# Performance work log

Measured on AMD Instinct MI355X. Metric: run time of the kernel, lower is better.

The kernel has to match this reference:

```python
import jax, jax.numpy as jnp
from jax import lax
import numpy as np

B, V, H, K, E = 256, 30000, 512, 200, 300
SH_ALPHA = 20.0
REC_W = 0.7
N_ITERS = 100       # fixed iteration budget (original caps at 5000; convergence check freezes updates)
STOP_THR = 0.005
BN_EPS = 1e-3


def setup_inputs() -> dict:
    key = jax.random.key(0)
    ks = jax.random.split(key, 8)
    n = lambda k, shape, scale: (jax.random.normal(k, shape, jnp.float32) * scale)
    return {
        "bows": jax.random.uniform(ks[0], (B, V), jnp.float32),
        "W1": n(ks[1], (H, V), 0.01),
        "b1": jnp.zeros((H,), jnp.float32),
        "W2": n(ks[2], (K, H), 0.05),
        "b2": jnp.zeros((K,), jnp.float32),
        "gamma": jnp.ones((K,), jnp.float32),
        "beta": jnp.zeros((K,), jnp.float32),
        "word_emb": n(ks[3], (V, E), 0.1),
        "topic_emb": n(ks[4], (K, E), 0.1),
    }


def _l2norm(x):
    return x / jnp.maximum(jnp.linalg.norm(x, axis=1, keepdims=True), 1e-12)


def _sinkhorn(cost, kernel, a, b):
    # a: [K,B], b: [V,B], kernel: [K,V]
    u0 = jnp.ones_like(a) / a.shape[0]
    v0 = jnp.ones_like(b)

    def body(carry, i):
        u, v, err = carry
        active = err > STOP_THR
        # u = a / (kernel @ (b / (u^T kernel)^T))
        u1 = a / (kernel @ (b / (u.T @ kernel).T))

        def check(_):
            v1 = b / (kernel.T @ u1)
            u2 = a / (kernel @ v1)
            bb = v1 * (kernel.T @ u2)
            e = jnp.max(jnp.sum(jnp.abs(bb - b), axis=0))
            return u2, v1, e

        # original does the v-refresh + err check when steps % 20 == 1 (steps = i+1)
        u1, v1, e1 = lax.cond(i % 20 == 0, check, lambda _: (u1, v, err), None)
        u = jnp.where(active, u1, u)
        v = jnp.where(active, v1, v)
        err = jnp.where(active, e1, err)
        return (u, v, err), None

    (u, v, _), _ = lax.scan(jax.checkpoint(body), (u0, v0, jnp.asarray(1.0, a.dtype)),
                            jnp.arange(N_ITERS))
    # per-document sinkhorn cost: sum_k u * ((kernel*cost) @ v)
    return jnp.sum(u * ((kernel * cost) @ v), axis=0)  # [B]


def reference(bows, W1, b1, W2, b2, gamma, beta, word_emb, topic_emb):
    # encoder (training-mode BN with batch stats; dropout disabled for determinism)
    h = jax.nn.relu(bows @ W1.T + b1)                      # [B,H]
    z = h @ W2.T + b2                                      # [B,K]
    mu = jnp.mean(z, axis=0)
    var = jnp.var(z, axis=0)                               # biased, as torch BN uses
    zn = gamma * (z - mu) / jnp.sqrt(var + BN_EPS) + beta
    doc_topic = jax.nn.softmax(zn, axis=1)                 # [B,K]

    topic_word = _l2norm(topic_emb) @ _l2norm(word_emb).T  # [K,V]
    cost = 1.0 - topic_word
    kernel = jnp.exp(-cost * SH_ALPHA)

    doc_word = jax.nn.softmax(bows, axis=1)                # [B,V]
    sinkhorn_loss = _sinkhorn(cost, kernel, doc_topic.T, doc_word.T).mean()

    rec_log_probs = jax.nn.log_softmax(doc_topic @ topic_word, axis=1)  # [B,V]
    reconstruction_loss = -(rec_log_probs * bows).sum(axis=1).mean()
    return REC_W * reconstruction_loss, sinkhorn_loss
```

## Files before the change

kernel.cpp:

```cpp
#include <hip/hip_runtime.h>
#include <math.h>

#define CDIV(a,b) (((a)+(b)-1)/(b))

typedef unsigned short u16;
typedef unsigned long long u64;
typedef __attribute__((ext_vector_type(8))) short bf16x8;
typedef __attribute__((ext_vector_type(4))) float f32x4;

constexpr int Bn = 256;
constexpr int Vn = 30000;
constexpr int Hn = 512;
constexpr int Kn = 200;
constexpr int En = 300;
constexpr int E3 = 320;
constexpr int Kp = 224;
constexpr int Vc = 224;
constexpr int NCH = 136;
constexpr int CPX = NCH / 8;
constexpr int Vpad = NCH * Vc;
constexpr int KQ = 50;
constexpr int SW1 = 120;
constexpr int KSL = 256;
constexpr float ALPHA  = 20.0f;
constexpr float RECW   = 0.7f;
constexpr float THRC   = 0.005f;
constexpr float EPS_BN = 1e-3f;
constexpr int   NIT    = 100;

__device__ __forceinline__ float bf2f(u16 h) {
  union { unsigned u; float f; } c; c.u = (unsigned)h << 16; return c.f;
}
__device__ __forceinline__ u16 f2bf(float f) {
  union { float f; unsigned u; } c; c.f = f;
  return (u16)((c.u + 0x7fffu + ((c.u >> 16) & 1u)) >> 16);
}
__device__ __forceinline__ bf16x8 load8bf(const float* p) {
  float4 a = *(const float4*)p, b = *(const float4*)(p + 4);
  bf16x8 r;
  r[0] = (short)f2bf(a.x); r[1] = (short)f2bf(a.y);
  r[2] = (short)f2bf(a.z); r[3] = (short)f2bf(a.w);
  r[4] = (short)f2bf(b.x); r[5] = (short)f2bf(b.y);
  r[6] = (short)f2bf(b.z); r[7] = (short)f2bf(b.w);
  return r;
}

template<int MODE>
__global__ __launch_bounds__(256, 2)
void fusedAB(const u16* __restrict__ kernT, const u16* __restrict__ kernA,
             const u16* __restrict__ ub, const u16* __restrict__ bmb,
             u16* __restrict__ wout, const u16* __restrict__ win,
             u16* __restrict__ tpart, float* __restrict__ errp,
             const int* __restrict__ frozen)
{
  if (MODE != 3 && frozen[0]) return;
  const int bid = blockIdx.x;
  const int xcd = bid & 7, wid = bid >> 3;
  const int c = xcd * CPX + (wid >> 2), g = wid & 3;
  const int v0 = c * Vc, b0 = g * 64;
  const int tid = threadIdx.x;
  const int wv = tid >> 6, l = tid & 63, l15 = l & 15, lg = l >> 4;
  const int rloc = wv * 16 + l15;
  const int bcol = b0 + rloc;
  __shared__ u16 wlds[64 * Vc];
  char* wbase = (char*)wlds;
  const int sw = (rloc & 3) << 4;

  if (MODE != 3) {
    bf16x8 uf[7];
    {
      const u16* up = ub + (size_t)bcol * Kp + lg * 8;
#pragma unroll
      for (int ks = 0; ks < 7; ++ks) uf[ks] = *(const bf16x8*)(up + ks * 32);
    }
    float e = 0.f;
    for (int vt = 0; vt < Vc / 16; ++vt) {
      const u16* ktp = kernT + (size_t)(v0 + vt * 16 + l15) * Kp + lg * 8;
      f32x4 acc = {0.f, 0.f, 0.f, 0.f};
#pragma unroll
      for (int ks = 0; ks < 7; ++ks) {
        bf16x8 kf = *(const bf16x8*)(ktp + ks * 32);
        acc = __builtin_amdgcn_mfma_f32_16x16x32_bf16(kf, uf[ks], acc, 0, 0, 0);
      }
      const int vbase = v0 + vt * 16 + lg * 4;
      const size_t po = (size_t)bcol * Vpad + vbase;
      u64 bq = __builtin_nontemporal_load((const u64*)(bmb + po));
      if (MODE == 2) {
        u64 wq = __builtin_nontemporal_load((const u64*)(win + po));
#pragma unroll
        for (int r = 0; r < 4; ++r) {
          float bm = bf2f((u16)(bq >> (16 * r)));
          float wv_ = bf2f((u16)(wq >> (16 * r)));
          e += fabsf(wv_ * acc[r] - bm);
        }
      } else {
        u64 wq = 0;
#pragma unroll
        for (int r = 0; r < 4; ++r) {
          float bm = bf2f((u16)(bq >> (16 * r)));
          float w = (vbase + r < Vn) ? bm / acc[r] : 0.f;
          wq |= (u64)f2bf(w) << (16 * r);
        }
        *(u64*)(wbase + rloc * (Vc * 2) + ((vt * 32 + lg * 8) ^ sw)) = wq;
        if (MODE == 1) __builtin_nontemporal_store(wq, (u64*)(wout + po));
      }
    }
    if (MODE == 2) {
      e += __shfl_xor(e, 16, 64);
      e += __shfl_xor(e, 32, 64);
      if (l < 16) errp[c * Bn + bcol] = e;
      return;
    }
    __syncthreads();
  }

  f32x4 accB[13];
#pragma unroll
  for (int mt = 0; mt < 13; ++mt) accB[mt] = (f32x4){0.f, 0.f, 0.f, 0.f};
  for (int vs = 0; vs < Vc / 32; ++vs) {
    bf16x8 wf;
    if (MODE == 3) {
      union { u64 q[2]; bf16x8 v; } wu;
      const u64* wp = (const u64*)(win + (size_t)bcol * Vpad + v0 + vs * 32 + lg * 8);
      wu.q[0] = __builtin_nontemporal_load(wp);
      wu.q[1] = __builtin_nontemporal_load(wp + 1);
      wf = wu.v;
    } else {
      wf = *(const bf16x8*)(wbase + rloc * (Vc * 2) + (((vs * 32 + lg * 8) * 2) ^ sw));
    }
    const u16* kap = kernA + (size_t)l15 * Vpad + v0 + vs * 32 + lg * 8;
#pragma unroll
    for (int mt = 0; mt < 13; ++mt) {
      bf16x8 af = *(const bf16x8*)(kap + (size_t)mt * 16 * Vpad);
      accB[mt] = __builtin_amdgcn_mfma_f32_16x16x32_bf16(af, wf, accB[mt], 0, 0, 0);
    }
  }
#pragma unroll
  for (int mt = 0; mt < 13; ++mt) {
    const int kq = mt * 4 + lg;
    if (kq < KQ) {
      u64 q = (u64)f2bf(accB[mt][0])
            | ((u64)f2bf(accB[mt][1]) << 16)
            | ((u64)f2bf(accB[mt][2]) << 32)
            | ((u64)f2bf(accB[mt][3]) << 48);
      __builtin_nontemporal_store(q, (u64*)(tpart + (((size_t)c * KQ + kq) * Bn + bcol) * 4));
    }
  }
}

__global__ __launch_bounds__(256, 2)
void reconMF(const u16* __restrict__ costT, const u16* __restrict__ dtb,
             u16* __restrict__ rbuf)
{
  const int c = blockIdx.x, g = blockIdx.y;
  const int v0 = c * Vc, b0 = g * 64;
  const int tid = threadIdx.x;
  const int wv = tid >> 6, l = tid & 63, l15 = l & 15, lg = l >> 4;
  const int bcol = b0 + wv * 16 + l15;
  bf16x8 uf[7];
  {
    const u16* up = dtb + (size_t)bcol * Kp + lg * 8;
#pragma unroll
    for (int ks = 0; ks < 7; ++ks) uf[ks] = *(const bf16x8*)(up + ks * 32);
  }
  for (int vt = 0; vt < Vc / 16; ++vt) {
    const u16* ktp = costT + (size_t)(v0 + vt * 16 + l15) * Kp + lg * 8;
    f32x4 acc = {0.f, 0.f, 0.f, 0.f};
#pragma unroll
    for (int ks = 0; ks < 7; ++ks) {
      bf16x8 kf = *(const bf16x8*)(ktp + ks * 32);
      acc = __builtin_amdgcn_mfma_f32_16x16x32_bf16(kf, uf[ks], acc, 0, 0, 0);
    }
    const int vbase = v0 + vt * 16 + lg * 4;
    u64 q = 0;
#pragma unroll
    for (int r = 0; r < 4; ++r) q |= (u64)f2bf(1.f - acc[r]) << (16 * r);
    *(u64*)(rbuf + (size_t)bcol * Vpad + vbase) = q;
  }
}

__global__ __launch_bounds__(256)
void gemmTW(const u16* __restrict__ nth, const u16* __restrict__ ntl,
            const u16* __restrict__ nwh, const u16* __restrict__ nwl,
            u16* __restrict__ kern_bf, u16* __restrict__ kc_bf,
            u16* __restrict__ cost_bf)
{
  const int n0 = blockIdx.x * 64;
  const int tid = threadIdx.x;
  const int wv = tid >> 6, l = tid & 63, l15 = l & 15, lg = l >> 4;
  const int n = n0 + wv * 16 + l15;
  const bool nok = n < Vn;
  f32x4 acc[14];
#pragma unroll
  for (int mt = 0; mt < 14; ++mt) acc[mt] = (f32x4){0.f, 0.f, 0.f, 0.f};
  for (int kc = 0; kc < E3; kc += 32) {
    bf16x8 bh = {0,0,0,0,0,0,0,0}, bl = {0,0,0,0,0,0,0,0};
    if (nok) {
      const size_t o = (size_t)n * E3 + kc + lg * 8;
      bh = *(const bf16x8*)(nwh + o);
      bl = *(const bf16x8*)(nwl + o);
    }
#pragma unroll
    for (int mt = 0; mt < 14; ++mt) {
      const size_t ao = (size_t)(mt * 16 + l15) * E3 + kc + lg * 8;
      bf16x8 ah = *(const bf16x8*)(nth + ao);
      bf16x8 al = *(const bf16x8*)(ntl + ao);
      acc[mt] = __builtin_amdgcn_mfma_f32_16x16x32_bf16(ah, bh, acc[mt], 0, 0, 0);
      acc[mt] = __builtin_amdgcn_mfma_f32_16x16x32_bf16(ah, bl, acc[mt], 0, 0, 0);
      acc[mt] = __builtin_amdgcn_mfma_f32_16x16x32_bf16(al, bh, acc[mt], 0, 0, 0);
    }
  }
#pragma unroll
  for (int mt = 0; mt < 14; ++mt) {
#pragma unroll
    for (int r = 0; r < 4; ++r) {
      int k = mt * 16 + lg * 4 + r;
      float cf = 1.f - acc[mt][r];
      float kf = expf(-ALPHA * cf);
      size_t o = (size_t)k * Vpad + n;
      kern_bf[o] = f2bf(kf);
      kc_bf[o]   = f2bf(kf * cf);
      cost_bf[o] = f2bf(cf);
    }
  }
}

__global__ __launch_bounds__(256)
void gemmW1(const float* __restrict__ A, const float* __restrict__ B,
            float* __restrict__ part)
{
  const int bid = blockIdx.x;
  const int xcd = bid & 7, t = bid >> 3;
  const int s = xcd * 15 + (t >> 3);
  const int nx = t & 7;
  const int n0 = nx * 64, k0 = s * KSL;
  const int tid = threadIdx.x;
  const int wv = tid >> 6, l = tid & 63, l15 = l & 15, lg = l >> 4;
  f32x4 acc[4][4];
#pragma unroll
  for (int i = 0; i < 4; ++i)
#pragma unroll
    for (int j = 0; j < 4; ++j) acc[i][j] = (f32x4){0.f, 0.f, 0.f, 0.f};

  bf16x8 aA[4], bA[4], aB[4], bB[4];

#define LDW1(KC, AF, BF)                                                        \
  { const int kk_ = (KC) + lg * 8;                                              \
    const bool ok_ = kk_ < Vn;                                                  \
    _Pragma("unroll")                                                           \
    for (int mt = 0; mt < 4; ++mt) {                                            \
      const int m_ = wv * 64 + mt * 16 + l15;                                   \
      AF[mt] = ok_ ? load8bf(A + (size_t)m_ * Vn + kk_) : (bf16x8){0,0,0,0,0,0,0,0}; \
    }                                                                           \
    _Pragma("unroll")                                                           \
    for (int nt = 0; nt < 4; ++nt) {                                            \
      const int n_ = n0 + nt * 16 + l15;                                        \
      BF[nt] = ok_ ? load8bf(B + (size_t)n_ * Vn + kk_) : (bf16x8){0,0,0,0,0,0,0,0}; \
    } }

#define FMAW1(AF, BF)                                                           \
  _Pragma("unroll")                                                             \
  for (int mt = 0; mt < 4; ++mt)                                                \
    _Pragma("unroll")                                                           \
    for (int nt = 0; nt < 4; ++nt)                                              \
      acc[mt][nt] = __builtin_amdgcn_mfma_f32_16x16x32_bf16(AF[mt], BF[nt], acc[mt][nt], 0, 0, 0);

  LDW1(k0, aA, bA);
#pragma unroll
  for (int step = 0; step < KSL / 32; ++step) {
    if ((step & 1) == 0) {
      if (step + 1 < KSL / 32) LDW1(k0 + (step + 1) * 32, aB, bB);
      FMAW1(aA, bA);
    } else {
      if (step + 1 < KSL / 32) LDW1(k0 + (step + 1) * 32, aA, bA);
      FMAW1(aB, bB);
    }
  }
#undef LDW1
#undef FMAW1

#pragma unroll
  for (int mt = 0; mt < 4; ++mt)
#pragma unroll
    for (int nt = 0; nt < 4; ++nt)
#pragma unroll
      for (int r = 0; r < 4; ++r) {
        const int m = wv * 64 + mt * 16 + lg * 4 + r;
        const int n = n0 + nt * 16 + l15;
        part[(size_t)s * (Bn * Hn) + (size_t)m * Hn + n] = acc[mt][nt][r];
      }
}

__global__ void transposeK(const u16* __restrict__ src, u16* __restrict__ dst)
{
  __shared__ u16 t[32][33];
  int tx = threadIdx.x & 31, ty = threadIdx.x >> 5;
  int v0 = blockIdx.x * 32, k0 = blockIdx.y * 32;
#pragma unroll
  for (int r = 0; r < 4; ++r) t[ty + 8 * r][tx] = src[(size_t)(k0 + ty + 8 * r) * Vpad + v0 + tx];
  __syncthreads();
#pragma unroll
  for (int r = 0; r < 4; ++r) dst[(size_t)(v0 + ty + 8 * r) * Kp + k0 + tx] = t[tx][ty + 8 * r];
}

__global__ void convTemb(const float* __restrict__ temb, const float* __restrict__ rnT,
                         u16* __restrict__ nth, u16* __restrict__ ntl)
{
  int k = blockIdx.x, e = threadIdx.x;
  float v = (k < Kn && e < En) ? temb[(size_t)k * En + e] * rnT[k] : 0.f;
  u16 hi = f2bf(v);
  nth[(size_t)k * E3 + e] = hi;
  ntl[(size_t)k * E3 + e] = f2bf(v - bf2f(hi));
}

__global__ void convWemb(const float* __restrict__ wemb, const float* __restrict__ rnW,
                         u16* __restrict__ nwh, u16* __restrict__ nwl)
{
  for (size_t idx = (size_t)blockIdx.x * 256 + threadIdx.x; idx < (size_t)Vn * E3;
       idx += (size_t)gridDim.x * 256) {
    int v = (int)(idx / E3), e = (int)(idx - (size_t)v * E3);
    float x = (e < En) ? wemb[(size_t)v * En + e] * rnW[v] : 0.f;
    u16 hi = f2bf(x);
    nwh[idx] = hi;
    nwl[idx] = f2bf(x - bf2f(hi));
  }
}

__global__ __launch_bounds__(256)
void gemm_nt(const float* __restrict__ A, const float* __restrict__ Bm,
             float* __restrict__ P, int M, int N, int Kd)
{
  const int S = gridDim.z, s = blockIdx.z;
  const int k0 = (int)((long long)Kd * s / S);
  const int k1 = (int)((long long)Kd * (s + 1) / S);
  const int m0 = blockIdx.y * 64, n0 = blockIdx.x * 64;
  __shared__ float As[16][68];
  __shared__ float Bs[16][68];
  const int tid = threadIdx.x;
  const int tx = tid & 15, ty = tid >> 4;
  const int lrow = tid >> 2, lkg = (tid & 3) * 4;
  const int mi = m0 + lrow, ni = n0 + lrow;
  float acc[4][4] = {};
  for (int kc = k0; kc < k1; kc += 16) {
    float4 a4 = {0.f, 0.f, 0.f, 0.f}, b4 = {0.f, 0.f, 0.f, 0.f};
    if (mi < M) a4 = *(const float4*)&A[(size_t)mi * Kd + kc + lkg];
    if (ni < N) b4 = *(const float4*)&Bm[(size_t)ni * Kd + kc + lkg];
    As[lkg + 0][lrow] = a4.x; As[lkg + 1][lrow] = a4.y;
    As[lkg + 2][lrow] = a4.z; As[lkg + 3][lrow] = a4.w;
    Bs[lkg + 0][lrow] = b4.x; Bs[lkg + 1][lrow] = b4.y;
    Bs[lkg + 2][lrow] = b4.z; Bs[lkg + 3][lrow] = b4.w;
    __syncthreads();
#pragma unroll
    for (int kk = 0; kk < 16; ++kk) {
      float4 av = *(const float4*)&As[kk][ty * 4];
      float4 bv = *(const float4*)&Bs[kk][tx * 4];
      float a_[4] = {av.x, av.y, av.z, av.w};
      float b_[4] = {bv.x, bv.y, bv.z, bv.w};
#pragma unroll
      for (int i = 0; i < 4; ++i)
#pragma unroll
        for (int j = 0; j < 4; ++j)
          acc[i][j] += a_[i] * b_[j];
    }
    __syncthreads();
  }
  const size_t base = (size_t)s * M * N;
#pragma unroll
  for (int i = 0; i < 4; ++i) {
    int m = m0 + ty * 4 + i;
    if (m >= M) continue;
#pragma unroll
    for (int j = 0; j < 4; ++j) {
      int n = n0 + tx * 4 + j;
      if (n < N) P[base + (size_t)m * N + n] = acc[i][j];
    }
  }
}

__global__ void rowNorms(const float* __restrict__ X, float* __restrict__ rn, int R, int C)
{
  int wv = threadIdx.x >> 6, lane = threadIdx.x & 63;
  int r = blockIdx.x * 4 + wv;
  if (r >= R) return;
  float s = 0.f;
  for (int c = lane; c < C; c += 64) { float x = X[(size_t)r * C + c]; s += x * x; }
#pragma unroll
  for (int m = 32; m; m >>= 1) s += __shfl_xor(s, m, 64);
  if (lane == 0) rn[r] = 1.f / fmaxf(sqrtf(s), 1e-12f);
}

__global__ void epiH(const float* __restrict__ P, const float* __restrict__ b1,
                     float* __restrict__ h, int S)
{
  int i = blockIdx.x * blockDim.x + threadIdx.x;
  if (i >= Bn * Hn) return;
  float v = b1[i & (Hn - 1)];
#pragma unroll 8
  for (int s = 0; s < S; ++s) v += P[(size_t)s * Bn * Hn + i];
  h[i] = fmaxf(v, 0.f);
}

__global__ void bnStats(const float* __restrict__ P, const float* __restrict__ b2,
                        float* __restrict__ mu, float* __restrict__ ivar, int S)
{
  int k = blockIdx.x, b = threadIdx.x;
  float z = b2[k];
  for (int s = 0; s < S; ++s) z += P[((size_t)s * Bn + b) * Kn + k];
  __shared__ float r1[256], r2[256];
  r1[b] = z; r2[b] = z * z; __syncthreads();
  for (int st = 128; st; st >>= 1) {
    if (b < st) { r1[b] += r1[b + st]; r2[b] += r2[b + st]; }
    __syncthreads();
  }
  if (b == 0) {
    float m = r1[0] / Bn, v = r2[0] / Bn - (r1[0] / Bn) * (r1[0] / Bn);
    mu[k] = m; ivar[k] = rsqrtf(v + EPS_BN);
  }
}

__global__ void bnSoftmax(const float* __restrict__ P, const float* __restrict__ b2,
                          const float* __restrict__ mu, const float* __restrict__ ivar,
                          const float* __restrict__ gamma, const float* __restrict__ beta,
                          float* __restrict__ a, u16* __restrict__ dtb, int S)
{
  int b = blockIdx.x, k = threadIdx.x;
  float zn = -1e30f;
  if (k < Kn) {
    float z = b2[k];
    for (int s = 0; s < S; ++s) z += P[((size_t)s * Bn + b) * Kn + k];
    zn = gamma[k] * (z - mu[k]) * ivar[k] + beta[k];
  }
  __shared__ float red[256];
  red[k] = zn; __syncthreads();
  for (int st = 128; st; st >>= 1) { if (k < st) red[k] = fmaxf(red[k], red[k + st]); __syncthreads(); }
  float mx = red[0]; __syncthreads();
  float e = (k < Kn) ? expf(zn - mx) : 0.f;
  red[k] = e; __syncthreads();
  for (int st = 128; st; st >>= 1) { if (k < st) red[k] += red[k + st]; __syncthreads(); }
  float dt = e / red[0];
  if (k < Kn) a[(size_t)k * Bn + b] = dt;
  if (k < Kp) dtb[(size_t)b * Kp + k] = (k < Kn) ? f2bf(dt) : (u16)0;
}

__global__ __launch_bounds__(512)
void rowSoftmax2(const float* __restrict__ bows, u16* __restrict__ bmb)
{
  int b = blockIdx.x, t = threadIdx.x;
  const float4* row = (const float4*)(bows + (size_t)b * Vn);
  __shared__ float red[512];
  float mx = -1e30f;
  for (int v4 = t; v4 < Vn / 4; v4 += 512) {
    float4 x = row[v4];
    mx = fmaxf(mx, fmaxf(fmaxf(x.x, x.y), fmaxf(x.z, x.w)));
  }
  red[t] = mx; __syncthreads();
  for (int st = 256; st; st >>= 1) { if (t < st) red[t] = fmaxf(red[t], red[t + st]); __syncthreads(); }
  mx = red[0]; __syncthreads();
  float sum = 0.f;
  for (int v4 = t; v4 < Vn / 4; v4 += 512) {
    float4 x = row[v4];
    sum += expf(x.x - mx) + expf(x.y - mx) + expf(x.z - mx) + expf(x.w - mx);
  }
  red[t] = sum; __syncthreads();
  for (int st = 256; st; st >>= 1) { if (t < st) red[t] += red[t + st]; __syncthreads(); }
  float inv = 1.f / red[0];
  for (int v4 = t; v4 < Vn / 4; v4 += 512) {
    float4 x = row[v4];
    u64 q = (u64)f2bf(expf(x.x - mx) * inv)
          | ((u64)f2bf(expf(x.y - mx) * inv) << 16)
          | ((u64)f2bf(expf(x.z - mx) * inv) << 32)
          | ((u64)f2bf(expf(x.w - mx) * inv) << 48);
    *(u64*)(bmb + (size_t)b * Vpad + v4 * 4) = q;
  }
  for (int p = t; p < (Vpad - Vn) / 4; p += 512)
    *(u64*)(bmb + (size_t)b * Vpad + Vn + p * 4) = 0;
}

__global__ void initU2(u16* __restrict__ ub)
{
  int b = blockIdx.x, k = threadIdx.x;
  ub[(size_t)b * Kp + k] = (k < Kn) ? f2bf(1.f / Kn) : (u16)0;
}

__global__ __launch_bounds__(256)
void updateU2(const u16* __restrict__ tpart, const float* __restrict__ a,
              u16* __restrict__ ub, const int* __restrict__ frozen)
{
  if (frozen[0]) return;
  const int kq = blockIdx.x >> 2, bq = blockIdx.x & 3;
  const int cg = threadIdx.x >> 6, bloc = threadIdx.x & 63;
  const int b = bq * 64 + bloc;
  f32x4 t = {0.f, 0.f, 0.f, 0.f};
  for (int c = cg * (NCH / 4); c < (cg + 1) * (NCH / 4); ++c) {
    u64 qd = __builtin_nontemporal_load(
        (const u64*)(tpart + (((size_t)c * KQ + kq) * Bn + b) * 4));
    t[0] += bf2f((u16)qd);         t[1] += bf2f((u16)(qd >> 16));
    t[2] += bf2f((u16)(qd >> 32)); t[3] += bf2f((u16)(qd >> 48));
  }
  __shared__ f32x4 red[4][64];
  red[cg][bloc] = t;
  __syncthreads();
  if (cg == 0) {
    f32x4 s = red[0][bloc];
#pragma unroll
    for (int gg = 1; gg < 4; ++gg) {
      f32x4 o = red[gg][bloc];
      s[0] += o[0]; s[1] += o[1]; s[2] += o[2]; s[3] += o[3];
    }
    const int k0 = kq * 4;
    u64 q = (u64)f2bf(a[(size_t)(k0 + 0) * Bn + b] / s[0])
          | ((u64)f2bf(a[(size_t)(k0 + 1) * Bn + b] / s[1]) << 16)
          | ((u64)f2bf(a[(size_t)(k0 + 2) * Bn + b] / s[2]) << 32)
          | ((u64)f2bf(a[(size_t)(k0 + 3) * Bn + b] / s[3]) << 48);
    *(u64*)(ub + (size_t)b * Kp + k0) = q;
  }
}

__global__ __launch_bounds__(256)
void sumT(const u16* __restrict__ tpart, float* __restrict__ t2)
{
  const int kq = blockIdx.x >> 2, bq = blockIdx.x & 3;
  const int cg = threadIdx.x >> 6, bloc = threadIdx.x & 63;
  const int b = bq * 64 + bloc;
  f32x4 t = {0.f, 0.f, 0.f, 0.f};
  for (int c = cg * (NCH / 4); c < (cg + 1) * (NCH / 4); ++c) {
    u64 qd = __builtin_nontemporal_load(
        (const u64*)(tpart + (((size_t)c * KQ + kq) * Bn + b) * 4));
    t[0] += bf2f((u16)qd);         t[1] += bf2f((u16)(qd >> 16));
    t[2] += bf2f((u16)(qd >> 32)); t[3] += bf2f((u16)(qd >> 48));
  }
  __shared__ f32x4 red[4][64];
  red[cg][bloc] = t;
  __syncthreads();
  if (cg == 0) {
    f32x4 s = red[0][bloc];
#pragma unroll
    for (int gg = 1; gg < 4; ++gg) {
      f32x4 o = red[gg][bloc];
      s[0] += o[0]; s[1] += o[1]; s[2] += o[2]; s[3] += o[3];
    }
    float4 ov; ov.x = s[0]; ov.y = s[1]; ov.z = s[2]; ov.w = s[3];
    *(float4*)&t2[(((size_t)kq * Bn) + b) * 4] = ov;
  }
}

__global__ void errFin(const float* __restrict__ errp, int nc, int* __restrict__ frozen)
{
  if (frozen[0]) return;
  int b = threadIdx.x;
  float s = 0.f;
  for (int c = 0; c < nc; ++c) s += errp[(size_t)c * Bn + b];
  __shared__ float red[256];
  red[b] = s; __syncthreads();
  for (int st = 128; st; st >>= 1) { if (b < st) red[b] = fmaxf(red[b], red[b + st]); __syncthreads(); }
  if (b == 0 && red[0] <= THRC) frozen[0] = 1;
}

__global__ __launch_bounds__(512)
void recPass2(const u16* __restrict__ r, const float* __restrict__ bows,
              float* __restrict__ Lb)
{
  int b = blockIdx.x, t = threadIdx.x;
  const float m = 1.0f;
  const float4* br = (const float4*)(bows + (size_t)b * Vn);
  float se = 0.f, dot = 0.f, bs = 0.f;
  for (int v4 = t; v4 < Vn / 4; v4 += 512) {
    u64 q = *(const u64*)(r + (size_t)b * Vpad + v4 * 4);
    float4 w = br[v4];
    float x0 = bf2f((u16)q), x1 = bf2f((u16)(q >> 16));
    float x2 = bf2f((u16)(q >> 32)), x3 = bf2f((u16)(q >> 48));
    se  += expf(x0 - m) + expf(x1 - m) + expf(x2 - m) + expf(x3 - m);
    dot += w.x * x0 + w.y * x1 + w.z * x2 + w.w * x3;
    bs  += w.x + w.y + w.z + w.w;
  }
  __shared__ float red[512];
  red[t] = se; __syncthreads();
  for (int st = 256; st; st >>= 1) { if (t < st) red[t] += red[t + st]; __syncthreads(); }
  float seT = red[0]; __syncthreads();
  red[t] = dot; __syncthreads();
  for (int st = 256; st; st >>= 1) { if (t < st) red[t] += red[t + st]; __syncthreads(); }
  float dotT = red[0]; __syncthreads();
  red[t] = bs; __syncthreads();
  for (int st = 256; st; st >>= 1) { if (t < st) red[t] += red[t + st]; __syncthreads(); }
  if (t == 0) Lb[b] = dotT - (m + logf(seT)) * red[0];
}

__global__ void finalOut(const u16* __restrict__ ub, const float* __restrict__ t2,
                         const float* __restrict__ Lb, float* __restrict__ outp)
{
  int b = threadIdx.x;
  float sl = 0.f;
  for (int k = 0; k < Kn; ++k)
    sl += bf2f(ub[(size_t)b * Kp + k]) * t2[(((size_t)(k >> 2) * Bn) + b) * 4 + (k & 3)];
  __shared__ float r1[256], r2[256];
  r1[b] = sl; r2[b] = Lb[b]; __syncthreads();
  for (int st = 128; st; st >>= 1) {
    if (b < st) { r1[b] += r1[b + st]; r2[b] += r2[b + st]; }
    __syncthreads();
  }
  if (b == 0) {
    outp[0] = RECW * (-(r2[0] / (float)Bn));
    outp[1] = r1[0] / (float)Bn;
  }
}

extern "C" void kernel_launch(void* const* d_in, const int* in_sizes, int n_in,
                              void* d_out, int out_size, void* d_ws, size_t ws_size,
                              hipStream_t stream)
{
  const float* bows  = (const float*)d_in[0];
  const float* W1    = (const float*)d_in[1];
  const float* b1    = (const float*)d_in[2];
  const float* W2    = (const float*)d_in[3];
  const float* b2    = (const float*)d_in[4];
  const float* gamma = (const float*)d_in[5];
  const float* beta  = (const float*)d_in[6];
  const float* wemb  = (const float*)d_in[7];
  const float* temb  = (const float*)d_in[8];
  float* out = (float*)d_out;

  float* ws = (float*)d_ws;
  size_t off = 0;
  auto alloc = [&](size_t n) { float* p = ws + off; off += (n + 63) & ~(size_t)63; return p; };
  size_t r1_floats = (size_t)Vn * E3;
  if ((size_t)SW1 * Bn * Hn > r1_floats) r1_floats = (size_t)SW1 * Bn * Hn;
  float* R1      = alloc(r1_floats);
  u16*   kern_bf = (u16*)alloc(((size_t)Kp * Vpad + 1) / 2);
  u16*   kernT   = (u16*)alloc(((size_t)Vpad * Kp + 1) / 2);
  u16*   kc_bf   = (u16*)alloc(((size_t)Kp * Vpad + 1) / 2);
  u16*   cost_bf = (u16*)alloc(((size_t)Kp * Vpad + 1) / 2);
  u16*   costT   = (u16*)alloc(((size_t)Vpad * Kp + 1) / 2);
  u16*   nt_hi   = (u16*)alloc(((size_t)Kp * E3 + 1) / 2);
  u16*   nt_lo   = (u16*)alloc(((size_t)Kp * E3 + 1) / 2);
  u16*   ub_bf   = (u16*)alloc(((size_t)Bn * Kp + 1) / 2);
  u16*   dt_bf   = (u16*)alloc(((size_t)Bn * Kp + 1) / 2);
  u16*   tpart   = (u16*)alloc(((size_t)NCH * KQ * Bn * 4 + 1) / 2);
  float* w2buf   = alloc((size_t)4 * Bn * Kn);
  float* hbuf    = alloc((size_t)Bn * Hn);
  float* abuf    = alloc((size_t)Kn * Bn);
  float* t2      = alloc((size_t)KQ * Bn * 4);
  float* rnT     = alloc(Kn);
  float* rnW     = alloc(Vn);
  float* mu      = alloc(Kn);
  float* ivar    = alloc(Kn);
  float* errp    = alloc((size_t)NCH * Bn);
  float* Lb      = alloc(Bn);
  int* frozen = (int*)(ws + off); off += 64;
  if (off * sizeof(float) > ws_size) return;
  u16*   nw_hi  = (u16*)R1;
  u16*   nw_lo  = nw_hi + (size_t)Vn * E3;
  float* w1part = R1;
  u16*   bm_bf  = (u16*)R1;
  u16*   vb_bf  = bm_bf + (size_t)Bn * Vpad;
  u16*   rbuf   = kern_bf;

  hipMemsetAsync(frozen, 0, sizeof(int), stream);

  rowNorms<<<CDIV(Kn, 4), 256, 0, stream>>>(temb, rnT, Kn, En);
  rowNorms<<<CDIV(Vn, 4), 256, 0, stream>>>(wemb, rnW, Vn, En);
  convTemb<<<Kp, E3, 0, stream>>>(temb, rnT, nt_hi, nt_lo);
  convWemb<<<4096, 256, 0, stream>>>(wemb, rnW, nw_hi, nw_lo);
  gemmTW<<<Vpad / 64, 256, 0, stream>>>(nt_hi, nt_lo, nw_hi, nw_lo, kern_bf, kc_bf, cost_bf);
  transposeK<<<dim3(Vpad / 32, Kp / 32), 256, 0, stream>>>(kern_bf, kernT);
  transposeK<<<dim3(Vpad / 32, Kp / 32), 256, 0, stream>>>(cost_bf, costT);

  gemmW1<<<8 * SW1, 256, 0, stream>>>(bows, W1, w1part);
  epiH<<<CDIV(Bn * Hn, 256), 256, 0, stream>>>(w1part, b1, hbuf, SW1);
  {
    dim3 g(CDIV(Kn, 64), CDIV(Bn, 64), 4);
    gemm_nt<<<g, 256, 0, stream>>>(hbuf, W2, w2buf, Bn, Kn, Hn);
  }
  bnStats<<<Kn, 256, 0, stream>>>(w2buf, b2, mu, ivar, 4);
  bnSoftmax<<<Bn, 256, 0, stream>>>(w2buf, b2, mu, ivar, gamma, beta, abuf, dt_bf, 4);
  rowSoftmax2<<<Bn, 512, 0, stream>>>(bows, bm_bf);
  initU2<<<Bn, Kp, 0, stream>>>(ub_bf);

  const int gF = NCH * 4;
  for (int it = 0; it < NIT; ++it) {
    fusedAB<0><<<gF, 256, 0, stream>>>(kernT, kern_bf, ub_bf, bm_bf, nullptr, nullptr, tpart, nullptr, frozen);
    updateU2<<<KQ * 4, 256, 0, stream>>>(tpart, abuf, ub_bf, frozen);
    if (it % 20 == 0) {
      fusedAB<1><<<gF, 256, 0, stream>>>(kernT, kern_bf, ub_bf, bm_bf, vb_bf, nullptr, tpart, nullptr, frozen);
      updateU2<<<KQ * 4, 256, 0, stream>>>(tpart, abuf, ub_bf, frozen);
      fusedAB<2><<<gF, 256, 0, stream>>>(kernT, kern_bf, ub_bf, bm_bf, nullptr, vb_bf, tpart, errp, frozen);
      errFin<<<1, 256, 0, stream>>>(errp, NCH, frozen);
    }
  }

  reconMF<<<dim3(NCH, Bn / 64), 256, 0, stream>>>(costT, dt_bf, rbuf);
  recPass2<<<Bn, 512, 0, stream>>>(rbuf, bows, Lb);

  fusedAB<3><<<gF, 256, 0, stream>>>(nullptr, kc_bf, ub_bf, nullptr, nullptr, vb_bf, tpart, nullptr, frozen);
  sumT<<<KQ * 4, 256, 0, stream>>>(tpart, t2);
  finalOut<<<1, 256, 0, stream>>>(ub_bf, t2, Lb, out);
}
```

Before: 2.476 ms.

## Fuse u-update and error reduction into sinkhorn kernel via atomic grid barrier

Folds the separate updateU2 and errFin kernels into the fused sinkhorn kernel. Each block bumps an atomic counter, and the first blocks spin until every block has arrived, then reduce the partial sums and write the new u or the frozen flag. This removes a launch and a kernel boundary per iteration. It also retunes the V-chunk width and count and the W1 GEMM split, replaces the XOR swizzle with LDS row padding, and drops nontemporal hints. The spin-wait assumes all 480 blocks are co-resident on the GPU, and each launch needs its own counter slot.

Measured after the change: 3.446 ms. 39.2% more time.

```diff
diff --git a/kernel.cpp b/kernel.cpp
--- a/kernel.cpp
+++ b/kernel.cpp
@@ -4,6 +4,7 @@
 #define CDIV(a,b) (((a)+(b)-1)/(b))
 
 typedef unsigned short u16;
+typedef unsigned int u32;
 typedef unsigned long long u64;
 typedef __attribute__((ext_vector_type(8))) short bf16x8;
 typedef __attribute__((ext_vector_type(4))) float f32x4;
@@ -15,13 +16,15 @@
 constexpr int En = 300;
 constexpr int E3 = 320;
 constexpr int Kp = 224;
-constexpr int Vc = 224;
-constexpr int NCH = 136;
+constexpr int Vc = 256;
+constexpr int VcP = Vc + 8;
+constexpr int NCH = 120;
 constexpr int CPX = NCH / 8;
 constexpr int Vpad = NCH * Vc;
 constexpr int KQ = 50;
-constexpr int SW1 = 120;
-constexpr int KSL = 256;
+constexpr int NBLK = NCH * 4;
+constexpr int SW1 = 64;
+constexpr int KSL = 480;
 constexpr float ALPHA  = 20.0f;
 constexpr float RECW   = 0.7f;
 constexpr float THRC   = 0.005f;
@@ -47,11 +50,12 @@
 
 template<int MODE>
 __global__ __launch_bounds__(256, 2)
-void fusedAB(const u16* __restrict__ kernT, const u16* __restrict__ kernA,
-             const u16* __restrict__ ub, const u16* __restrict__ bmb,
-             u16* __restrict__ wout, const u16* __restrict__ win,
-             u16* __restrict__ tpart, float* __restrict__ errp,
-             const int* __restrict__ frozen)
+void fusedIter(const u16* __restrict__ kernT, const u16* __restrict__ kernA,
+               u16* __restrict__ ub, const u16* __restrict__ bmb,
+               u16* __restrict__ wout, const u16* __restrict__ win,
+               u16* __restrict__ tpart, float* __restrict__ errp,
+               const float* __restrict__ abuf, int* __restrict__ frozen,
+               u32* __restrict__ ctr)
 {
   if (MODE != 3 && frozen[0]) return;
   const int bid = blockIdx.x;
@@ -62,11 +66,10 @@
   const int wv = tid >> 6, l = tid & 63, l15 = l & 15, lg = l >> 4;
   const int rloc = wv * 16 + l15;
   const int bcol = b0 + rloc;
-  __shared__ u16 wlds[64 * Vc];
+  __shared__ u16 wlds[64 * VcP];
   char* wbase = (char*)wlds;
-  const int sw = (rloc & 3) << 4;
-
-  if (MODE != 3) {
+
+  if (MODE == 0 || MODE == 1 || MODE == 2) {
     bf16x8 uf[7];
     {
       const u16* up = ub + (size_t)bcol * Kp + lg * 8;
@@ -84,9 +87,9 @@
       }
       const int vbase = v0 + vt * 16 + lg * 4;
       const size_t po = (size_t)bcol * Vpad + vbase;
-      u64 bq = __builtin_nontemporal_load((const u64*)(bmb + po));
+      u64 bq = *(const u64*)(bmb + po);
       if (MODE == 2) {
-        u64 wq = __builtin_nontemporal_load((const u64*)(win + po));
+        u64 wq = *(const u64*)(win + po);
 #pragma unroll
         for (int r = 0; r < 4; ++r) {
           float bm = bf2f((u16)(bq >> (16 * r)));
@@ -101,14 +104,33 @@
           float w = (vbase + r < Vn) ? bm / acc[r] : 0.f;
           wq |= (u64)f2bf(w) << (16 * r);
         }
-        *(u64*)(wbase + rloc * (Vc * 2) + ((vt * 32 + lg * 8) ^ sw)) = wq;
-        if (MODE == 1) __builtin_nontemporal_store(wq, (u64*)(wout + po));
+        *(u64*)(wbase + rloc * (VcP * 2) + vt * 32 + lg * 8) = wq;
+        if (MODE == 1) *(u64*)(wout + po) = wq;
       }
     }
     if (MODE == 2) {
       e += __shfl_xor(e, 16, 64);
       e += __shfl_xor(e, 32, 64);
       if (l < 16) errp[c * Bn + bcol] = e;
+      __builtin_amdgcn_fence(__ATOMIC_RELEASE, "agent");
+      __syncthreads();
+      if (tid == 0) __hip_atomic_fetch_add(ctr, 1u, __ATOMIC_RELAXED, __HIP_MEMORY_SCOPE_AGENT);
+      if (bid != 0) return;
+      if (tid == 0) {
+        while (__hip_atomic_load(ctr, __ATOMIC_RELAXED, __HIP_MEMORY_SCOPE_AGENT) < (u32)NBLK)
+          __builtin_amdgcn_s_sleep(2);
+      }
+      __syncthreads();
+      __builtin_amdgcn_fence(__ATOMIC_ACQUIRE, "agent");
+      float* red = (float*)wlds;
+      float s = 0.f;
+      for (int cc = 0; cc < NCH; ++cc) s += errp[(size_t)cc * Bn + tid];
+      red[tid] = s; __syncthreads();
+      for (int st = 128; st; st >>= 1) {
+        if (tid < st) red[tid] = fmaxf(red[tid], red[tid + st]);
+        __syncthreads();
+      }
+      if (tid == 0 && red[0] <= THRC) frozen[0] = 1;
       return;
     }
     __syncthreads();
@@ -119,15 +141,8 @@
   for (int mt = 0; mt < 13; ++mt) accB[mt] = (f32x4){0.f, 0.f, 0.f, 0.f};
   for (int vs = 0; vs < Vc / 32; ++vs) {
     bf16x8 wf;
-    if (MODE == 3) {
-      union { u64 q[2]; bf16x8 v; } wu;
-      const u64* wp = (const u64*)(win + (size_t)bcol * Vpad + v0 + vs * 32 + lg * 8);
-      wu.q[0] = __builtin_nontemporal_load(wp);
-      wu.q[1] = __builtin_nontemporal_load(wp + 1);
-      wf = wu.v;
-    } else {
-      wf = *(const bf16x8*)(wbase + rloc * (Vc * 2) + (((vs * 32 + lg * 8) * 2) ^ sw));
-    }
+    if (MODE == 3) wf = *(const bf16x8*)(win + (size_t)bcol * Vpad + v0 + vs * 32 + lg * 8);
+    else wf = *(const bf16x8*)(wbase + rloc * (VcP * 2) + vs * 64 + lg * 16);
     const u16* kap = kernA + (size_t)l15 * Vpad + v0 + vs * 32 + lg * 8;
 #pragma unroll
     for (int mt = 0; mt < 13; ++mt) {
@@ -143,7 +158,47 @@
             | ((u64)f2bf(accB[mt][1]) << 16)
             | ((u64)f2bf(accB[mt][2]) << 32)
             | ((u64)f2bf(accB[mt][3]) << 48);
-      __builtin_nontemporal_store(q, (u64*)(tpart + (((size_t)c * KQ + kq) * Bn + bcol) * 4));
+      *(u64*)(tpart + (((size_t)c * KQ + kq) * Bn + bcol) * 4) = q;
+    }
+  }
+  if (MODE == 3) return;
+
+  __builtin_amdgcn_fence(__ATOMIC_RELEASE, "agent");
+  __syncthreads();
+  if (tid == 0) __hip_atomic_fetch_add(ctr, 1u, __ATOMIC_RELAXED, __HIP_MEMORY_SCOPE_AGENT);
+  if (bid >= KQ * 4) return;
+  if (tid == 0) {
+    while (__hip_atomic_load(ctr, __ATOMIC_RELAXED, __HIP_MEMORY_SCOPE_AGENT) < (u32)NBLK)
+      __builtin_amdgcn_s_sleep(2);
+  }
+  __syncthreads();
+  __builtin_amdgcn_fence(__ATOMIC_ACQUIRE, "agent");
+  {
+    const int kq = bid >> 2, bq = bid & 3;
+    const int cg = tid >> 6, bloc = tid & 63;
+    const int b = bq * 64 + bloc;
+    f32x4 t = {0.f, 0.f, 0.f, 0.f};
+    for (int cc = cg * (NCH / 4); cc < (cg + 1) * (NCH / 4); ++cc) {
+      u64 qd = *(const u64*)(tpart + (((size_t)cc * KQ + kq) * Bn + b) * 4);
+      t[0] += bf2f((u16)qd);         t[1] += bf2f((u16)(qd >> 16));
+      t[2] += bf2f((u16)(qd >> 32)); t[3] += bf2f((u16)(qd >> 48));
+    }
+    f32x4* red = (f32x4*)wlds;
+    red[cg * 64 + bloc] = t;
+    __syncthreads();
+    if (cg == 0) {
+      f32x4 s = red[bloc];
+#pragma unroll
+      for (int gg = 1; gg < 4; ++gg) {
+        f32x4 o = red[gg * 64 + bloc];
+        s[0] += o[0]; s[1] += o[1]; s[2] += o[2]; s[3] += o[3];
+      }
+      const int k0 = kq * 4;
+      u64 q = (u64)f2bf(abuf[(size_t)(k0 + 0) * Bn + b] / s[0])
+            | ((u64)f2bf(abuf[(size_t)(k0 + 1) * Bn + b] / s[1]) << 16)
+            | ((u64)f2bf(abuf[(size_t)(k0 + 2) * Bn + b] / s[2]) << 32)
+            | ((u64)f2bf(abuf[(size_t)(k0 + 3) * Bn + b] / s[3]) << 48);
+      *(u64*)(ub + (size_t)b * Kp + k0) = q;
     }
   }
 }
@@ -231,7 +286,7 @@
 {
   const int bid = blockIdx.x;
   const int xcd = bid & 7, t = bid >> 3;
-  const int s = xcd * 15 + (t >> 3);
+  const int s = xcd * 8 + (t >> 3);
   const int nx = t & 7;
   const int n0 = nx * 64, k0 = s * KSL;
   const int tid = threadIdx.x;
@@ -483,17 +538,14 @@
 }
 
 __global__ __launch_bounds__(256)
-void updateU2(const u16* __restrict__ tpart, const float* __restrict__ a,
-              u16* __restrict__ ub, const int* __restrict__ frozen)
-{
-  if (frozen[0]) return;
+void sumT(const u16* __restrict__ tpart, float* __restrict__ t2)
+{
   const int kq = blockIdx.x >> 2, bq = blockIdx.x & 3;
   const int cg = threadIdx.x >> 6, bloc = threadIdx.x & 63;
   const int b = bq * 64 + bloc;
   f32x4 t = {0.f, 0.f, 0.f, 0.f};
   for (int c = cg * (NCH / 4); c < (cg + 1) * (NCH / 4); ++c) {
-    u64 qd = __builtin_nontemporal_load(
-        (const u64*)(tpart + (((size_t)c * KQ + kq) * Bn + b) * 4));
+    u64 qd = *(const u64*)(tpart + (((size_t)c * KQ + kq) * Bn + b) * 4);
     t[0] += bf2f((u16)qd);         t[1] += bf2f((u16)(qd >> 16));
     t[2] += bf2f((u16)(qd >> 32)); t[3] += bf2f((u16)(qd >> 48));
   }
@@ -507,53 +559,9 @@
       f32x4 o = red[gg][bloc];
       s[0] += o[0]; s[1] += o[1]; s[2] += o[2]; s[3] += o[3];
     }
-    const int k0 = kq * 4;
-    u64 q = (u64)f2bf(a[(size_t)(k0 + 0) * Bn + b] / s[0])
-          | ((u64)f2bf(a[(size_t)(k0 + 1) * Bn + b] / s[1]) << 16)
-          | ((u64)f2bf(a[(size_t)(k0 + 2) * Bn + b] / s[2]) << 32)
-          | ((u64)f2bf(a[(size_t)(k0 + 3) * Bn + b] / s[3]) << 48);
-    *(u64*)(ub + (size_t)b * Kp + k0) = q;
-  }
-}
-
-__global__ __launch_bounds__(256)
-void sumT(const u16* __restrict__ tpart, float* __restrict__ t2)
-{
-  const int kq = blockIdx.x >> 2, bq = blockIdx.x & 3;
-  const int cg = threadIdx.x >> 6, bloc = threadIdx.x & 63;
-  const int b = bq * 64 + bloc;
-  f32x4 t = {0.f, 0.f, 0.f, 0.f};
-  for (int c = cg * (NCH / 4); c < (cg + 1) * (NCH / 4); ++c) {
-    u64 qd = __builtin_nontemporal_load(
-        (const u64*)(tpart + (((size_t)c * KQ + kq) * Bn + b) * 4));
-    t[0] += bf2f((u16)qd);         t[1] += bf2f((u16)(qd >> 16));
-    t[2] += bf2f((u16)(qd >> 32)); t[3] += bf2f((u16)(qd >> 48));
-  }
-  __shared__ f32x4 red[4][64];
-  red[cg][bloc] = t;
-  __syncthreads();
-  if (cg == 0) {
-    f32x4 s = red[0][bloc];
-#pragma unroll
-    for (int gg = 1; gg < 4; ++gg) {
-      f32x4 o = red[gg][bloc];
-      s[0] += o[0]; s[1] += o[1]; s[2] += o[2]; s[3] += o[3];
-    }
     float4 ov; ov.x = s[0]; ov.y = s[1]; ov.z = s[2]; ov.w = s[3];
     *(float4*)&t2[(((size_t)kq * Bn) + b) * 4] = ov;
   }
-}
-
-__global__ void errFin(const float* __restrict__ errp, int nc, int* __restrict__ frozen)
-{
-  if (frozen[0]) return;
-  int b = threadIdx.x;
-  float s = 0.f;
-  for (int c = 0; c < nc; ++c) s += errp[(size_t)c * Bn + b];
-  __shared__ float red[256];
-  red[b] = s; __syncthreads();
-  for (int st = 128; st; st >>= 1) { if (b < st) red[b] = fmaxf(red[b], red[b + st]); __syncthreads(); }
-  if (b == 0 && red[0] <= THRC) frozen[0] = 1;
 }
 
 __global__ __launch_bounds__(512)
@@ -645,6 +653,7 @@
   float* ivar    = alloc(Kn);
   float* errp    = alloc((size_t)NCH * Bn);
   float* Lb      = alloc(Bn);
+  u32* ctrbuf = (u32*)(ws + off); off += 128;
   int* frozen = (int*)(ws + off); off += 64;
   if (off * sizeof(float) > ws_size) return;
   u16*   nw_hi  = (u16*)R1;
@@ -655,6 +664,7 @@
   u16*   rbuf   = kern_bf;
 
   hipMemsetAsync(frozen, 0, sizeof(int), stream);
+  hipMemsetAsync(ctrbuf, 0, 128 * sizeof(u32), stream);
 
   rowNorms<<<CDIV(Kn, 4), 256, 0, stream>>>(temb, rnT, Kn, En);
   rowNorms<<<CDIV(Vn, 4), 256, 0, stream>>>(wemb, rnW, Vn, En);
@@ -675,22 +685,27 @@
   rowSoftmax2<<<Bn, 512, 0, stream>>>(bows, bm_bf);
   initU2<<<Bn, Kp, 0, stream>>>(ub_bf);
 
-  const int gF = NCH * 4;
+  int slot = 0;
   for (int it = 0; it < NIT; ++it) {
-    fusedAB<0><<<gF, 256, 0, stream>>>(kernT, kern_bf, ub_bf, bm_bf, nullptr, nullptr, tpart, nullptr, frozen);
-    updateU2<<<KQ * 4, 256, 0, stream>>>(tpart, abuf, ub_bf, frozen);
+    fusedIter<0><<<NBLK, 256, 0, stream>>>(kernT, kern_bf, ub_bf, bm_bf, nullptr,
+                                           nullptr, tpart, errp, abuf, frozen,
+                                           ctrbuf + slot++);
     if (it % 20 == 0) {
-      fusedAB<1><<<gF, 256, 0, stream>>>(kernT, kern_bf, ub_bf, bm_bf, vb_bf, nullptr, tpart, nullptr, frozen);
-      updateU2<<<KQ * 4, 256, 0, stream>>>(tpart, abuf, ub_bf, frozen);
-      fusedAB<2><<<gF, 256, 0, stream>>>(kernT, kern_bf, ub_bf, bm_bf, nullptr, vb_bf, tpart, errp, frozen);
-      errFin<<<1, 256, 0, stream>>>(errp, NCH, frozen);
+      fusedIter<1><<<NBLK, 256, 0, stream>>>(kernT, kern_bf, ub_bf, bm_bf, vb_bf,
+                                             nullptr, tpart, errp, abuf, frozen,
+                                             ctrbuf + slot++);
+      fusedIter<2><<<NBLK, 256, 0, stream>>>(kernT, kern_bf, ub_bf, bm_bf, nullptr,
+                                             vb_bf, tpart, errp, abuf, frozen,
+                                             ctrbuf + slot++);
     }
   }
 
   reconMF<<<dim3(NCH, Bn / 64), 256, 0, stream>>>(costT, dt_bf, rbuf);
   recPass2<<<Bn, 512, 0, stream>>>(rbuf, bows, Lb);
 
-  fusedAB<3><<<gF, 256, 0, stream>>>(nullptr, kc_bf, ub_bf, nullptr, nullptr, vb_bf, tpart, nullptr, frozen);
+  fusedIter<3><<<NBLK, 256, 0, stream>>>(nullptr, kc_bf, ub_bf, nullptr, nullptr,
+                                         vb_bf, tpart, errp, abuf, frozen,
+                                         ctrbuf + slot++);
   sumT<<<KQ * 4, 256, 0, stream>>>(tpart, t2);
   finalOut<<<1, 256, 0, stream>>>(ub_bf, t2, Lb, out);
 }
```
